# Optimization experiments

Hardware: AMD Instinct MI355X
Metric: run time of the kernel (lower is better)

The kernel has to match this reference:

```python
import math
import jax, jax.numpy as jnp
import numpy as np


def setup_inputs() -> dict:
    key = jax.random.key(0)
    k1, k2 = jax.random.split(key)
    N, H, W, h, d = 32, 32, 32, 16, 64
    input_NHWhd = jax.random.normal(k1, (N, H, W, h, d), dtype=jnp.float32)
    emb_2dd = jax.random.uniform(k2, (2, d, d), dtype=jnp.float32) * (2.0 * math.pi)
    return {"input_NHWhd": input_NHWhd, "emb_2dd": emb_2dd}


def _positions(H, W):
    # xlim = sqrt(W/H), ylim = sqrt(H/W); positions stacked as (y, x)
    xlim = math.sqrt(W / H)
    ylim = math.sqrt(H / W)
    x_HW = jnp.broadcast_to(jnp.linspace(-xlim, xlim, W, dtype=jnp.float32)[None, :], (H, W))
    y_HW = jnp.broadcast_to(jnp.linspace(-ylim, ylim, H, dtype=jnp.float32)[:, None], (H, W))
    return jnp.stack((y_HW, x_HW), axis=-1)  # [H, W, 2]


def reference(input_NHWhd, emb_2dd):
    N, H, W, h, d = input_NHWhd.shape
    # skew-symmetric generator bases (the -0.5 shift cancels in M - M^T,
    # kept for faithfulness to the original)
    upper_2dd = jnp.triu(emb_2dd, k=1) - 0.5
    skew_2dd = upper_2dd - jnp.swapaxes(upper_2dd, -2, -1)  # [2, d, d]
    pos_HW2 = _positions(H, W)
    # per-position generator: sum over the 2 spatial components
    gen_HWdd = jnp.einsum("hwc,cij->hwij", pos_HW2, skew_2dd)  # [H, W, d, d]
    rot_HWdd = jax.vmap(jax.scipy.linalg.expm)(gen_HWdd.reshape(-1, d, d)).reshape(H, W, d, d)
    # apply rotation: out[n,y,x,q,:] = input[n,y,x,q,:] @ rot[y,x]
    out_NHWhd = jnp.einsum("nhwqd,hwde->nhwqe", input_NHWhd, rot_HWdd.astype(input_NHWhd.dtype))
    return out_NHWhd
```

## Files before the change

kernel.cpp:

```cpp
#include <hip/hip_runtime.h>


typedef float f4 __attribute__((ext_vector_type(4)));
typedef short s8v __attribute__((ext_vector_type(8)));
typedef float f32x4 __attribute__((ext_vector_type(4)));

constexpr int LST = 68;
constexpr int BST = 72;

static __device__ __forceinline__ unsigned short f2bf(float f) {
    unsigned int u = __float_as_uint(f);
    u += 0x7fffu + ((u >> 16) & 1u);
    return (unsigned short)(u >> 16);
}

static __device__ __forceinline__ void mm(float* __restrict__ C,
                                          const float* __restrict__ A,
                                          const float* __restrict__ B,
                                          float cI, int tid) {
    const int r0 = (tid >> 4) << 2;
    const int c0 = (tid & 15) << 2;
    f4 acc0 = {0.f, 0.f, 0.f, 0.f}, acc1 = acc0, acc2 = acc0, acc3 = acc0;
#pragma unroll 4
    for (int k = 0; k < 64; k += 4) {
        f4 b0 = *(const f4*)&B[(k + 0) * LST + c0];
        f4 b1 = *(const f4*)&B[(k + 1) * LST + c0];
        f4 b2 = *(const f4*)&B[(k + 2) * LST + c0];
        f4 b3 = *(const f4*)&B[(k + 3) * LST + c0];
        f4 a0 = *(const f4*)&A[(r0 + 0) * LST + k];
        f4 a1 = *(const f4*)&A[(r0 + 1) * LST + k];
        f4 a2 = *(const f4*)&A[(r0 + 2) * LST + k];
        f4 a3 = *(const f4*)&A[(r0 + 3) * LST + k];
        acc0 += a0.x * b0; acc0 += a0.y * b1; acc0 += a0.z * b2; acc0 += a0.w * b3;
        acc1 += a1.x * b0; acc1 += a1.y * b1; acc1 += a1.z * b2; acc1 += a1.w * b3;
        acc2 += a2.x * b0; acc2 += a2.y * b1; acc2 += a2.z * b2; acc2 += a2.w * b3;
        acc3 += a3.x * b0; acc3 += a3.y * b1; acc3 += a3.z * b2; acc3 += a3.w * b3;
    }
    if (r0 == c0) { acc0.x += cI; acc1.y += cI; acc2.z += cI; acc3.w += cI; }
    *(f4*)&C[(r0 + 0) * LST + c0] = acc0;
    *(f4*)&C[(r0 + 1) * LST + c0] = acc1;
    *(f4*)&C[(r0 + 2) * LST + c0] = acc2;
    *(f4*)&C[(r0 + 3) * LST + c0] = acc3;
}

__global__ __launch_bounds__(256, 2)
void liere_fused(const float* __restrict__ in, const float* __restrict__ emb,
                 float* __restrict__ out) {
    __shared__ __align__(16) float sA[64 * LST];
    __shared__ __align__(16) float sU[64 * LST];
    __shared__ __align__(16) float sV[64 * LST];
    __shared__ float snorm;

    const int tid = threadIdx.x;
    const int p = blockIdx.x;
    const int y = p >> 5;
    const int x = p & 31;

#pragma unroll
    for (int i = 0; i < 4; ++i) {
        int lin = i * 1024 + tid * 4;
        int r = lin >> 6, c = lin & 63;
        *(f4*)&sU[r * LST + c] = *(const f4*)&emb[lin];
        *(f4*)&sV[r * LST + c] = *(const f4*)&emb[4096 + lin];
    }
    __syncthreads();

    const float yv = (2.0f * (float)y - 31.0f) / 31.0f;
    const float xv = (2.0f * (float)x - 31.0f) / 31.0f;
    {
        const int r0 = (tid >> 4) << 2, c0 = (tid & 15) << 2;
#pragma unroll
        for (int i = 0; i < 4; ++i)
#pragma unroll
            for (int j = 0; j < 4; ++j) {
                int r = r0 + i, c = c0 + j;
                float s0, s1;
                if (r < c)      { s0 = sU[r * LST + c];  s1 = sV[r * LST + c]; }
                else if (r > c) { s0 = -sU[c * LST + r]; s1 = -sV[c * LST + r]; }
                else            { s0 = 0.f; s1 = 0.f; }
                sA[r * LST + c] = yv * s0 + xv * s1;
            }
    }
    __syncthreads();

    if (tid < 64) {
        float s = 0.f;
        for (int c = 0; c < 64; ++c) s += fabsf(sA[tid * LST + c]);
#pragma unroll
        for (int off = 32; off > 0; off >>= 1) s = fmaxf(s, __shfl_down(s, off, 64));
        if (tid == 0) snorm = s;
    }
    __syncthreads();
    int sq = 0;
    {
        float nm = snorm;
        if (nm > 1.0f) sq = (int)ceilf(log2f(nm));
        if (sq < 0) sq = 0;
        if (sq > 14) sq = 14;
    }
    const float scale = exp2f((float)(-sq));

    const float C9 = 2.75573192e-6f, C8 = 2.48015876e-5f, C7 = 1.98412701e-4f,
                C6 = 1.38888893e-3f, C5 = 8.33333377e-3f, C4 = 4.16666679e-2f,
                C3 = 0.166666672f,   C2 = 0.5f,           C1 = 1.0f, C0 = 1.0f;

    {
        const int r0 = (tid >> 4) << 2, c0 = (tid & 15) << 2;
#pragma unroll
        for (int i = 0; i < 4; ++i)
#pragma unroll
            for (int j = 0; j < 4; ++j) {
                int r = r0 + i, c = c0 + j;
                float a = sA[r * LST + c] * scale;
                sA[r * LST + c] = a;
                sU[r * LST + c] = C9 * a + ((r == c) ? C8 : 0.f);
            }
    }
    __syncthreads();

    mm(sV, sU, sA, C7, tid); __syncthreads();
    mm(sU, sV, sA, C6, tid); __syncthreads();
    mm(sV, sU, sA, C5, tid); __syncthreads();
    mm(sU, sV, sA, C4, tid); __syncthreads();
    mm(sV, sU, sA, C3, tid); __syncthreads();
    mm(sU, sV, sA, C2, tid); __syncthreads();
    mm(sV, sU, sA, C1, tid); __syncthreads();
    mm(sU, sV, sA, C0, tid); __syncthreads();

    float* cur = sU;
    float* oth = sV;
    for (int i = 0; i < sq; ++i) {
        mm(oth, cur, cur, 0.f, tid);
        __syncthreads();
        float* t = cur; cur = oth; oth = t;
    }

    unsigned short* RT = (unsigned short*)sA;
    unsigned short* AS = (unsigned short*)(sA + 2304);

    const int w = tid >> 6;
    const int lane = tid & 63;
    const int m = lane & 15;
    const int q4 = lane >> 4;

    for (int pass = 0; pass < 2; ++pass) {
        __syncthreads();
        {
            int c = tid >> 2;
            int k0 = (tid & 3) << 4;
            for (int k = k0; k < k0 + 16; ++k) {
                float v = pass ? cur[c * LST + k] : cur[k * LST + c];
                RT[c * BST + k] = f2bf(v);
            }
        }
        __syncthreads();

        const int yy = pass ? (31 - y) : y;
        const int xx = pass ? (31 - x) : x;

        for (int n = 0; n < 32; ++n) {
            const size_t off = ((size_t)((n * 32 + yy) * 32 + xx)) * 1024;
            const float* src = in + off;
            float* dst = out + off;

            {
                f4 v = *(const f4*)(src + tid * 4);
                int q = tid >> 4, col = (tid & 15) << 2;
                unsigned int lo = (unsigned int)f2bf(v.x) | ((unsigned int)f2bf(v.y) << 16);
                unsigned int hi = (unsigned int)f2bf(v.z) | ((unsigned int)f2bf(v.w) << 16);
                unsigned int* d2 = (unsigned int*)&AS[q * BST + col];
                d2[0] = lo;
                d2[1] = hi;
            }
            __syncthreads();

            {
                const s8v a0 = *(const s8v*)&AS[m * BST + q4 * 8];
                const s8v a1 = *(const s8v*)&AS[m * BST + 32 + q4 * 8];
                const s8v b0 = *(const s8v*)&RT[(w * 16 + m) * BST + q4 * 8];
                const s8v b1 = *(const s8v*)&RT[(w * 16 + m) * BST + 32 + q4 * 8];
                f32x4 acc = {0.f, 0.f, 0.f, 0.f};
                acc = __builtin_amdgcn_mfma_f32_16x16x32_bf16(a0, b0, acc, 0, 0, 0);
                acc = __builtin_amdgcn_mfma_f32_16x16x32_bf16(a1, b1, acc, 0, 0, 0);
#pragma unroll
                for (int r = 0; r < 4; ++r)
                    dst[(q4 * 4 + r) * 64 + w * 16 + m] = acc[r];
            }
            __syncthreads();
        }
    }
}

extern "C" void kernel_launch(void* const* d_in, const int* in_sizes, int n_in,
                              void* d_out, int out_size, void* d_ws, size_t ws_size,
                              hipStream_t stream) {
    (void)in_sizes; (void)n_in; (void)out_size; (void)d_ws; (void)ws_size;
    const float* in = (const float*)d_in[0];
    const float* emb = (const float*)d_in[1];
    float* out = (float*)d_out;
    hipLaunchKernelGGL(liere_fused, dim3(512), dim3(256), 0, stream, in, emb, out);
}
```

Baseline: 303.1 us.

## Split passes and batch across waves, keep rotation fragments in registers

The apply phase previously ran the two passes one after the other, staging each input tile through shared memory with two block barriers per batch element. Now each wave owns one pass and half of the batch. The rotation operand is preloaded into registers once, and input rows are loaded straight from global into MFMA operands, computing the transposed product so each lane stores contiguous float4 outputs. This removes the per-iteration barriers and LDS traffic and gives wider stores, at the cost of more registers and a precomputed transposed bf16 copy of the rotation.

```diff
diff --git a/kernel.cpp b/kernel.cpp
--- a/kernel.cpp
+++ b/kernel.cpp
@@ -135,59 +135,75 @@
         float* t = cur; cur = oth; oth = t;
     }
 
-    unsigned short* RT = (unsigned short*)sA;
-    unsigned short* AS = (unsigned short*)(sA + 2304);
+    unsigned short* Rb = (unsigned short*)sA;
+    unsigned short* RT = (unsigned short*)oth;
+    {
+        const int r = tid >> 2;
+        const int k0 = (tid & 3) << 4;
+        for (int k = k0; k < k0 + 16; ++k) {
+            unsigned short b = f2bf(cur[r * LST + k]);
+            Rb[r * BST + k] = b;
+            RT[k * BST + r] = b;
+        }
+    }
+    __syncthreads();
 
     const int w = tid >> 6;
     const int lane = tid & 63;
     const int m = lane & 15;
     const int q4 = lane >> 4;
-
-    for (int pass = 0; pass < 2; ++pass) {
-        __syncthreads();
-        {
-            int c = tid >> 2;
-            int k0 = (tid & 3) << 4;
-            for (int k = k0; k < k0 + 16; ++k) {
-                float v = pass ? cur[c * LST + k] : cur[k * LST + c];
-                RT[c * BST + k] = f2bf(v);
-            }
-        }
-        __syncthreads();
-
-        const int yy = pass ? (31 - y) : y;
-        const int xx = pass ? (31 - x) : x;
-
-        for (int n = 0; n < 32; ++n) {
-            const size_t off = ((size_t)((n * 32 + yy) * 32 + xx)) * 1024;
-            const float* src = in + off;
-            float* dst = out + off;
-
-            {
-                f4 v = *(const f4*)(src + tid * 4);
-                int q = tid >> 4, col = (tid & 15) << 2;
-                unsigned int lo = (unsigned int)f2bf(v.x) | ((unsigned int)f2bf(v.y) << 16);
-                unsigned int hi = (unsigned int)f2bf(v.z) | ((unsigned int)f2bf(v.w) << 16);
-                unsigned int* d2 = (unsigned int*)&AS[q * BST + col];
-                d2[0] = lo;
-                d2[1] = hi;
-            }
-            __syncthreads();
-
-            {
-                const s8v a0 = *(const s8v*)&AS[m * BST + q4 * 8];
-                const s8v a1 = *(const s8v*)&AS[m * BST + 32 + q4 * 8];
-                const s8v b0 = *(const s8v*)&RT[(w * 16 + m) * BST + q4 * 8];
-                const s8v b1 = *(const s8v*)&RT[(w * 16 + m) * BST + 32 + q4 * 8];
-                f32x4 acc = {0.f, 0.f, 0.f, 0.f};
-                acc = __builtin_amdgcn_mfma_f32_16x16x32_bf16(a0, b0, acc, 0, 0, 0);
-                acc = __builtin_amdgcn_mfma_f32_16x16x32_bf16(a1, b1, acc, 0, 0, 0);
-#pragma unroll
-                for (int r = 0; r < 4; ++r)
-                    dst[(q4 * 4 + r) * 64 + w * 16 + m] = acc[r];
-            }
-            __syncthreads();
-        }
+    const int pass = w >> 1;
+    const int nbase = (w & 1) << 4;
+
+    const unsigned short* RF = pass ? Rb : RT;
+    s8v rf[4][2];
+#pragma unroll
+    for (int t = 0; t < 4; ++t) {
+        rf[t][0] = *(const s8v*)&RF[(t * 16 + m) * BST + q4 * 8];
+        rf[t][1] = *(const s8v*)&RF[(t * 16 + m) * BST + 32 + q4 * 8];
+    }
+
+    const int yy = pass ? (31 - y) : y;
+    const int xx = pass ? (31 - x) : x;
+    const size_t pos = (size_t)(yy * 32 + xx) * 1024;
+
+    for (int i = 0; i < 16; ++i) {
+        const int n = nbase + i;
+        const size_t nb = (size_t)n << 20;
+        const float* src = in + nb + pos + m * 64 + q4 * 8;
+        f4 u0 = *(const f4*)src;
+        f4 u1 = *(const f4*)(src + 4);
+        f4 u2 = *(const f4*)(src + 32);
+        f4 u3 = *(const f4*)(src + 36);
+        s8v b0, b1;
+        b0[0] = (short)f2bf(u0.x); b0[1] = (short)f2bf(u0.y);
+        b0[2] = (short)f2bf(u0.z); b0[3] = (short)f2bf(u0.w);
+        b0[4] = (short)f2bf(u1.x); b0[5] = (short)f2bf(u1.y);
+        b0[6] = (short)f2bf(u1.z); b0[7] = (short)f2bf(u1.w);
+        b1[0] = (short)f2bf(u2.x); b1[1] = (short)f2bf(u2.y);
+        b1[2] = (short)f2bf(u2.z); b1[3] = (short)f2bf(u2.w);
+        b1[4] = (short)f2bf(u3.x); b1[5] = (short)f2bf(u3.y);
+        b1[6] = (short)f2bf(u3.z); b1[7] = (short)f2bf(u3.w);
+
+        f32x4 acc0 = {0.f,0.f,0.f,0.f}, acc1 = acc0, acc2 = acc0, acc3 = acc0;
+        acc0 = __builtin_amdgcn_mfma_f32_16x16x32_bf16(rf[0][0], b0, acc0, 0, 0, 0);
+        acc0 = __builtin_amdgcn_mfma_f32_16x16x32_bf16(rf[0][1], b1, acc0, 0, 0, 0);
+        acc1 = __builtin_amdgcn_mfma_f32_16x16x32_bf16(rf[1][0], b0, acc1, 0, 0, 0);
+        acc1 = __builtin_amdgcn_mfma_f32_16x16x32_bf16(rf[1][1], b1, acc1, 0, 0, 0);
+        acc2 = __builtin_amdgcn_mfma_f32_16x16x32_bf16(rf[2][0], b0, acc2, 0, 0, 0);
+        acc2 = __builtin_amdgcn_mfma_f32_16x16x32_bf16(rf[2][1], b1, acc2, 0, 0, 0);
+        acc3 = __builtin_amdgcn_mfma_f32_16x16x32_bf16(rf[3][0], b0, acc3, 0, 0, 0);
+        acc3 = __builtin_amdgcn_mfma_f32_16x16x32_bf16(rf[3][1], b1, acc3, 0, 0, 0);
+
+        float* dst = out + nb + pos + m * 64 + q4 * 4;
+        f4 o0 = {acc0[0], acc0[1], acc0[2], acc0[3]};
+        f4 o1 = {acc1[0], acc1[1], acc1[2], acc1[3]};
+        f4 o2 = {acc2[0], acc2[1], acc2[2], acc2[3]};
+        f4 o3 = {acc3[0], acc3[1], acc3[2], acc3[3]};
+        *(f4*)(dst +  0) = o0;
+        *(f4*)(dst + 16) = o1;
+        *(f4*)(dst + 32) = o2;
+        *(f4*)(dst + 48) = o3;
     }
 }
 
```

Result: faster. 280.0 us (-7.6%).
